# Kernel tuning notes

Hardware: AMD Instinct MI355X
Metric: run time of the kernel (lower is better)

## Reference

```python
import jax, jax.numpy as jnp
import numpy as np

B, S, E, H, L, V = 2, 2048, 512, 8, 4, 10000
D = E // H  # head_dim = 64


def _linear(x, W, b):
    # torch nn.Linear: y = x @ W.T + b, W: [out, in]
    return jnp.einsum('bse,oe->bso', x, W) + b


def _layernorm(x, g, b, eps=1e-5):
    mu = jnp.mean(x, axis=-1, keepdims=True)
    var = jnp.mean((x - mu) ** 2, axis=-1, keepdims=True)
    return (x - mu) * jax.lax.rsqrt(var + eps) * g + b


def _mha(x, Wq, bq, Wk, bk, Wv, bv, Wo, bo):
    q = _linear(x, Wq, bq).reshape(B, S, H, D).transpose(0, 2, 1, 3)
    k = _linear(x, Wk, bk).reshape(B, S, H, D).transpose(0, 2, 1, 3)
    v = _linear(x, Wv, bv).reshape(B, S, H, D).transpose(0, 2, 1, 3)
    energy = jnp.einsum('bhqd,bhkd->bhqk', q, k)  # full [B,H,S,S] scores (faithful)
    attn = jax.nn.softmax(energy / jnp.sqrt(jnp.asarray(D, x.dtype)), axis=-1)
    out = jnp.einsum('bhqk,bhkd->bhqd', attn, v)
    out = out.transpose(0, 2, 1, 3).reshape(B, S, E)
    return _linear(out, Wo, bo)


def setup_inputs() -> dict:
    key = jax.random.key(0)
    ks = jax.random.split(key, 12)
    s = 0.02
    f32 = jnp.float32
    return {
        'tokens': jax.random.randint(ks[0], (B, S), 0, V, dtype=jnp.int32),
        'embed_table': jax.random.normal(ks[1], (V, E), f32) * s,
        'pos_enc': jax.random.normal(ks[2], (1, S, E), f32) * s,
        'Wq': jax.random.normal(ks[3], (L, E, E), f32) * s,
        'bq': jnp.zeros((L, E), f32),
        'Wk': jax.random.normal(ks[4], (L, E, E), f32) * s,
        'bk': jnp.zeros((L, E), f32),
        'Wv': jax.random.normal(ks[5], (L, E, E), f32) * s,
        'bv': jnp.zeros((L, E), f32),
        'Wo': jax.random.normal(ks[6], (L, E, E), f32) * s,
        'bo': jnp.zeros((L, E), f32),
        'ln_g': jnp.ones((L, E), f32),
        'ln_b': jnp.zeros((L, E), f32),
        'Wout': jax.random.normal(ks[7], (V, E), f32) * s,
        'bout': jnp.zeros((V,), f32),
    }


def reference(tokens, embed_table, pos_enc, Wq, bq, Wk, bk, Wv, bv, Wo, bo, ln_g, ln_b, Wout, bout):
    x = embed_table[tokens] + pos_enc[:, :S, :]
    for l in range(L):
        a = _mha(x, Wq[l], bq[l], Wk[l], bk[l], Wv[l], bv[l], Wo[l], bo[l])
        x = _layernorm(x + a, ln_g[l], ln_b[l])
    # NOTE: original module defines feed_forward but never calls it in forward()
    return jnp.einsum('bse,ve->bsv', x, Wout) + bout
```

## Files before the change

### kernel.cpp

```cpp
#include <hip/hip_runtime.h>
#include <hip/hip_bf16.h>

#define Bc 2
#define Sc 2048
#define Ec 512
#define Hc 8
#define Lc 4
#define Vc 10000
#define Dc 64
#define Mc (Bc*Sc)
#define NPAD 10112
#define NROWS (16*Sc)
#define SPLITS 2

typedef __hip_bfloat16 bf16;
typedef __attribute__((ext_vector_type(8))) short frag_ab;
typedef __attribute__((ext_vector_type(4))) float frag_cd;
typedef __attribute__((ext_vector_type(16))) float f32x16;

typedef __attribute__((address_space(3))) void lds_t;
typedef __attribute__((address_space(1))) void gm_t;
static __device__ __forceinline__ void gload16(const void* g, void* l) {
  __builtin_amdgcn_global_load_lds((const gm_t*)g, (lds_t*)l, 16, 0, 0);
}
static __device__ __forceinline__ frag_ab ldfrag(const bf16* p) {
  return *(const frag_ab*)p;
}
static __device__ __forceinline__ unsigned cvtpk(float lo, float hi) {
  unsigned w;
  asm("v_cvt_pk_bf16_f32 %0, %1, %2" : "=v"(w) : "v"(lo), "v"(hi));
  return w;
}

#define SCALE2 0.18033688011112042f

#define NQKV (Lc*1536*512)
#define NO   (Lc*512*512)
#define NOUT (NPAD*512)
__global__ void convert_kernel(const float* __restrict__ Wq, const float* __restrict__ Wk,
                               const float* __restrict__ Wv, const float* __restrict__ Wo,
                               const float* __restrict__ Wout,
                               bf16* __restrict__ wqkv, bf16* __restrict__ wo,
                               bf16* __restrict__ wout) {
  long i4 = (long)(blockIdx.x * 256 + threadIdx.x) * 4;
  if (i4 >= NQKV + NO + NOUT) return;
  float4 v;
  bf16* dst;
  if (i4 < NQKV) {
    int row = (int)(i4 >> 9), colb = (int)(i4 & 511);
    int l = row / 1536, rr = row - l * 1536;
    int seg = rr >> 9, r = rr & 511;
    const float* src = (seg == 0 ? Wq : seg == 1 ? Wk : Wv) + (((long)(l * 512 + r)) << 9) + colb;
    v = *(const float4*)src;
    dst = wqkv + i4;
  } else if (i4 < NQKV + NO) {
    long j = i4 - NQKV;
    v = *(const float4*)(Wo + j);
    dst = wo + j;
  } else {
    long j = i4 - NQKV - NO;
    int row = (int)(j >> 9);
    if (row < Vc) v = *(const float4*)(Wout + j);
    else { v.x = 0.f; v.y = 0.f; v.z = 0.f; v.w = 0.f; }
    dst = wout + j;
  }
  union { bf16 h[4]; short4 s4; } u;
  u.h[0] = __float2bfloat16(v.x);
  u.h[1] = __float2bfloat16(v.y);
  u.h[2] = __float2bfloat16(v.z);
  u.h[3] = __float2bfloat16(v.w);
  *(short4*)dst = u.s4;
}

__global__ void embed_kernel(const int* __restrict__ tok, const float* __restrict__ emb,
                             const float* __restrict__ pos, float* __restrict__ x,
                             bf16* __restrict__ xb) {
  int i = blockIdx.x * 256 + threadIdx.x;
  int row = i >> 9, c = i & 511;
  int s = row & (Sc - 1);
  float v = emb[tok[row] * Ec + c] + pos[s * Ec + c];
  x[i] = v;
  xb[i] = __float2bfloat16(v);
}

template<int MODE>
__global__ __launch_bounds__(256)
void gemm_tile(const bf16* __restrict__ A, const bf16* __restrict__ W,
               const float* __restrict__ b0, const float* __restrict__ b1,
               const float* __restrict__ b2,
               void* __restrict__ o0, void* __restrict__ o1, void* __restrict__ o2) {
  __shared__ bf16 As[128 * 32];
  __shared__ bf16 Bs[128 * 32];
  const int t = threadIdx.x;
  const int lane = t & 63;
  const int wv = t >> 6;
  const int c = lane & 15, quad = lane >> 4;
  const int m0 = blockIdx.x * 128, n0 = blockIdx.y * 128;
  const int wm = (wv & 1) * 64, wn = (wv >> 1) * 64;
  frag_cd acc[4][4] = {};

  const int p0 = t, p1 = t + 256;
  const int r0 = p0 >> 2, g0 = (p0 & 3) ^ ((r0 >> 1) & 3);
  const int r1 = p1 >> 2, g1 = (p1 & 3) ^ ((r1 >> 1) & 3);
  const bf16* a0 = A + (m0 + r0) * Ec + g0 * 8;
  const bf16* a1 = A + (m0 + r1) * Ec + g1 * 8;
  const bf16* w0 = W + (n0 + r0) * Ec + g0 * 8;
  const bf16* w1 = W + (n0 + r1) * Ec + g1 * 8;

  const int sw8 = ((quad ^ ((c >> 1) & 3))) * 8;

  for (int k = 0; k < Ec; k += 32) {
    __syncthreads();
    gload16(a0 + k, As + p0 * 8);
    gload16(a1 + k, As + p1 * 8);
    gload16(w0 + k, Bs + p0 * 8);
    gload16(w1 + k, Bs + p1 * 8);
    __syncthreads();
    frag_ab af[4], bfr[4];
#pragma unroll
    for (int i = 0; i < 4; ++i)
      af[i] = *(const frag_ab*)(As + (wm + i * 16 + c) * 32 + sw8);
#pragma unroll
    for (int j = 0; j < 4; ++j)
      bfr[j] = *(const frag_ab*)(Bs + (wn + j * 16 + c) * 32 + sw8);
#pragma unroll
    for (int i = 0; i < 4; ++i)
#pragma unroll
      for (int j = 0; j < 4; ++j)
        acc[i][j] = __builtin_amdgcn_mfma_f32_16x16x32_bf16(af[i], bfr[j], acc[i][j], 0, 0, 0);
  }

#pragma unroll
  for (int j = 0; j < 4; ++j) {
    int gn = n0 + wn + j * 16 + c;
    if (MODE == 0) {
      int seg = gn >> 9, col = gn & 511;
      const float* bp = seg == 0 ? b0 : seg == 1 ? b1 : b2;
      float bias = bp[col];
      int hh = col >> 6, dd = col & 63;
#pragma unroll
      for (int i = 0; i < 4; ++i)
#pragma unroll
        for (int ii = 0; ii < 4; ++ii) {
          int gm = m0 + wm + i * 16 + quad * 4 + ii;
          int bb = gm >> 11, ss = gm & (Sc - 1);
          float v = acc[i][j][ii] + bias;
          if (seg == 0)
            ((bf16*)o0)[((((bb << 3) + hh) * Sc + ss) << 6) + dd] = __float2bfloat16(v * SCALE2);
          else if (seg == 1)
            ((bf16*)o1)[((((bb << 3) + hh) * Sc + ss) << 6) + dd] = __float2bfloat16(v);
          else
            ((bf16*)o2)[((((bb << 3) + hh) << 6) + dd) * Sc + ss] = __float2bfloat16(v);
        }
    } else if (MODE == 1) {
      float bias = b0[gn];
#pragma unroll
      for (int i = 0; i < 4; ++i)
#pragma unroll
        for (int ii = 0; ii < 4; ++ii) {
          int gm = m0 + wm + i * 16 + quad * 4 + ii;
          ((float*)o0)[((long)gm << 9) + gn] = acc[i][j][ii] + bias;
        }
    } else {
      if (gn < Vc) {
        float bias = b0[gn];
#pragma unroll
        for (int i = 0; i < 4; ++i)
#pragma unroll
          for (int ii = 0; ii < 4; ++ii) {
            int gm = m0 + wm + i * 16 + quad * 4 + ii;
            ((float*)o0)[(long)gm * Vc + gn] = acc[i][j][ii] + bias;
          }
      }
    }
  }
}

__global__ __launch_bounds__(256, 2)
void attn_kernel(const bf16* __restrict__ Q, const bf16* __restrict__ Kb,
                 const bf16* __restrict__ Vt,
                 float* __restrict__ Op, float* __restrict__ lp) {
  __shared__ bf16 Ks[2][64 * 64];
  __shared__ bf16 Vs[2][64 * 64];
  const int t = threadIdx.x;
  const int lane = t & 63, wv = t >> 6;
  const int col = lane & 31, hi = lane >> 5;
  const int col7 = col & 7;

  int wg = (blockIdx.x & 7) * 64 + (blockIdx.x >> 3);
  const int bh = wg >> 5;
  const int split = (wg >> 4) & 1;
  const int q0 = (wg & 15) * 128 + wv * 32;

  const bf16* kbase = Kb + (long)bh * Sc * Dc + (long)(split << 10) * Dc;
  const bf16* vbase = Vt + (long)bh * Dc * Sc + (split << 10);

  const int p0 = t;
  const int r0 = p0 >> 3, c0 = (p0 & 7) ^ (r0 & 7);
  const bf16* ksrc0 = kbase + r0 * Dc + c0 * 8;
  const bf16* vsrc0 = vbase + r0 * Sc + c0 * 8;

  const bf16* qp = Q + ((long)bh * Sc + q0 + col) * Dc + hi * 8;
  frag_ab qf[4];
#pragma unroll
  for (int ck = 0; ck < 4; ++ck) qf[ck] = ldfrag(qp + ck * 16);

  f32x16 o0 = {}, o1 = {};
  float lsum = 0.f;

  gload16(ksrc0, Ks[0] + p0 * 8);
  gload16(ksrc0 + 32 * Dc, Ks[0] + (p0 + 256) * 8);
  gload16(vsrc0, Vs[0] + p0 * 8);
  gload16(vsrc0 + 32 * Sc, Vs[0] + (p0 + 256) * 8);

  for (int tI = 0; tI < 16; ++tI) {
    const int cur = tI & 1;
    if (tI < 15) {
      const int k0 = (tI + 1) * 64;
      bf16* kd = Ks[cur ^ 1];
      bf16* vd = Vs[cur ^ 1];
      gload16(ksrc0 + k0 * Dc, kd + p0 * 8);
      gload16(ksrc0 + (k0 + 32) * Dc, kd + (p0 + 256) * 8);
      gload16(vsrc0 + k0, vd + p0 * 8);
      gload16(vsrc0 + k0 + 32 * Sc, vd + (p0 + 256) * 8);
      asm volatile("s_waitcnt vmcnt(4)" ::: "memory");
    } else {
      asm volatile("s_waitcnt vmcnt(0)" ::: "memory");
    }
    __builtin_amdgcn_s_barrier();
    asm volatile("" ::: "memory");

    const bf16* KsB = Ks[cur];
    const bf16* VsB = Vs[cur];

    f32x16 st0 = {}, st1 = {};
#pragma unroll
    for (int ck = 0; ck < 4; ++ck) {
      frag_ab kf0 = ldfrag(KsB + col * 64 + (((2 * ck + hi) ^ col7) << 3));
      frag_ab kf1 = ldfrag(KsB + (32 + col) * 64 + (((2 * ck + hi) ^ col7) << 3));
      st0 = __builtin_amdgcn_mfma_f32_32x32x16_bf16(kf0, qf[ck], st0, 0, 0, 0);
      st1 = __builtin_amdgcn_mfma_f32_32x32x16_bf16(kf1, qf[ck], st1, 0, 0, 0);
    }

    float pa0[16], pa1[16];
    float ls = 0.f;
#pragma unroll
    for (int r = 0; r < 16; ++r) {
      pa0[r] = exp2f(st0[r]);
      pa1[r] = exp2f(st1[r]);
      ls += pa0[r] + pa1[r];
    }
    lsum += ls;

#pragma unroll
    for (int sj = 0; sj < 4; ++sj) {
      const float* pp = (sj < 2) ? pa0 : pa1;
      const int b8 = (sj & 1) * 8;
      unsigned cw0 = cvtpk(pp[b8 + 0], pp[b8 + 1]);
      unsigned cw1 = cvtpk(pp[b8 + 2], pp[b8 + 3]);
      unsigned cw2 = cvtpk(pp[b8 + 4], pp[b8 + 5]);
      unsigned cw3 = cvtpk(pp[b8 + 6], pp[b8 + 7]);
      auto r20 = __builtin_amdgcn_permlane32_swap((int)cw2, (int)cw0, false, false);
      auto r31 = __builtin_amdgcn_permlane32_swap((int)cw3, (int)cw1, false, false);
      union { unsigned u[4]; frag_ab f; } pa;
      pa.u[0] = (unsigned)r20[1];
      pa.u[1] = (unsigned)r31[1];
      pa.u[2] = (unsigned)r20[0];
      pa.u[3] = (unsigned)r31[0];
      frag_ab vf0 = ldfrag(VsB + col * 64 + (((2 * sj + hi) ^ col7) << 3));
      frag_ab vf1 = ldfrag(VsB + (32 + col) * 64 + (((2 * sj + hi) ^ col7) << 3));
      o0 = __builtin_amdgcn_mfma_f32_32x32x16_bf16(pa.f, vf0, o0, 0, 0, 0);
      o1 = __builtin_amdgcn_mfma_f32_32x32x16_bf16(pa.f, vf1, o1, 0, 0, 0);
    }

    asm volatile("" ::: "memory");
    __builtin_amdgcn_s_barrier();
  }

  const long rbase = (long)split * NROWS + (long)bh * Sc + q0;
  float ltot = lsum + __shfl_xor(lsum, 32, 64);
  if (lane < 32) lp[rbase + col] = ltot;
#pragma unroll
  for (int r = 0; r < 16; ++r) {
    int qr = (r & 3) + 8 * (r >> 2) + 4 * hi;
    Op[(rbase + qr) * Dc + col]      = o0[r];
    Op[(rbase + qr) * Dc + col + 32] = o1[r];
  }
}

__global__ void combine_kernel(const float* __restrict__ Op, const float* __restrict__ lp,
                               bf16* __restrict__ O) {
  int t = blockIdx.x * 256 + threadIdx.x;
  int d = (t & 31) * 2, r = t >> 5;
  int bh = r >> 11, ss = r & (Sc - 1);
  float2 a = *(const float2*)(Op + (long)r * Dc + d);
  float2 b = *(const float2*)(Op + (long)(NROWS + r) * Dc + d);
  float inv = 1.f / (lp[r] + lp[NROWS + r]);
  union { bf16 h[2]; unsigned u; } u2;
  u2.h[0] = __float2bfloat16((a.x + b.x) * inv);
  u2.h[1] = __float2bfloat16((a.y + b.y) * inv);
  int bb = bh >> 3, hh = bh & 7;
  *(unsigned*)&O[((long)bb * Sc + ss) * Ec + hh * Dc + d] = u2.u;
}

__global__ void ln_kernel(const float* __restrict__ x, const float* __restrict__ a,
                          const float* __restrict__ g, const float* __restrict__ bb,
                          float* __restrict__ xo, bf16* __restrict__ xbo) {
  int lane = threadIdx.x & 63, wv = threadIdx.x >> 6;
  int row = blockIdx.x * 4 + wv;
  const float* xr = x + (long)row * Ec;
  const float* ar = a + (long)row * Ec;
  float v[8];
  float sum = 0.f;
#pragma unroll
  for (int j = 0; j < 8; ++j) {
    int c = lane + j * 64;
    v[j] = xr[c] + ar[c];
    sum += v[j];
  }
#pragma unroll
  for (int d = 1; d < 64; d <<= 1) sum += __shfl_xor(sum, d, 64);
  float mu = sum * (1.f / 512.f);
  float sq = 0.f;
#pragma unroll
  for (int j = 0; j < 8; ++j) { float t = v[j] - mu; sq += t * t; }
#pragma unroll
  for (int d = 1; d < 64; d <<= 1) sq += __shfl_xor(sq, d, 64);
  float rs = 1.f / sqrtf(sq * (1.f / 512.f) + 1e-5f);
#pragma unroll
  for (int j = 0; j < 8; ++j) {
    int c = lane + j * 64;
    float y = (v[j] - mu) * rs * g[c] + bb[c];
    xo[(long)row * Ec + c] = y;
    xbo[(long)row * Ec + c] = __float2bfloat16(y);
  }
}

extern "C" void kernel_launch(void* const* d_in, const int* in_sizes, int n_in,
                              void* d_out, int out_size, void* d_ws, size_t ws_size,
                              hipStream_t stream) {
  const int*   tokens = (const int*)d_in[0];
  const float* embed  = (const float*)d_in[1];
  const float* pos    = (const float*)d_in[2];
  const float* Wq     = (const float*)d_in[3];
  const float* bq     = (const float*)d_in[4];
  const float* Wk     = (const float*)d_in[5];
  const float* bk     = (const float*)d_in[6];
  const float* Wv     = (const float*)d_in[7];
  const float* bv     = (const float*)d_in[8];
  const float* Wo     = (const float*)d_in[9];
  const float* bo     = (const float*)d_in[10];
  const float* ln_g   = (const float*)d_in[11];
  const float* ln_b   = (const float*)d_in[12];
  const float* Wout   = (const float*)d_in[13];
  const float* bout   = (const float*)d_in[14];
  float* out = (float*)d_out;

  char* ws = (char*)d_ws;
  size_t off = 0;
  float* x_f    = (float*)(ws + off); off += (size_t)Mc * Ec * 4;
  bf16*  xb     = (bf16*)(ws + off);  off += (size_t)Mc * Ec * 2;
  float* a_f    = (float*)(ws + off); off += (size_t)Mc * Ec * 4;
  bf16*  qb     = (bf16*)(ws + off);  off += (size_t)Mc * Ec * 2;
  bf16*  kb     = (bf16*)(ws + off);  off += (size_t)Mc * Ec * 2;
  bf16*  vtb    = (bf16*)(ws + off);  off += (size_t)Mc * Ec * 2;
  bf16*  attnb  = (bf16*)(ws + off);  off += (size_t)Mc * Ec * 2;
  bf16*  wqkv_b = (bf16*)(ws + off);  off += (size_t)NQKV * 2;
  bf16*  wo_b   = (bf16*)(ws + off);  off += (size_t)NO * 2;
  bf16*  wout_b = (bf16*)(ws + off);  off += (size_t)NOUT * 2;
  float* op_f   = (float*)(ws + off); off += (size_t)SPLITS * NROWS * Dc * 4;
  float* lp_f   = (float*)(ws + off); off += (size_t)SPLITS * NROWS * 4;

  int nconv = (NQKV + NO + NOUT) / 4;
  convert_kernel<<<(nconv + 255) / 256, 256, 0, stream>>>(Wq, Wk, Wv, Wo, Wout,
                                                          wqkv_b, wo_b, wout_b);

  embed_kernel<<<(Mc * Ec) / 256, 256, 0, stream>>>(tokens, embed, pos, x_f, xb);

  dim3 gqkv(Mc / 128, 1536 / 128);
  dim3 go(Mc / 128, Ec / 128);
  for (int l = 0; l < Lc; ++l) {
    const bf16* wqkv_l = wqkv_b + (size_t)l * 1536 * Ec;
    const bf16* wo_l   = wo_b + (size_t)l * Ec * Ec;
    gemm_tile<0><<<gqkv, 256, 0, stream>>>(xb, wqkv_l, bq + l * Ec, bk + l * Ec,
                                           bv + l * Ec, qb, kb, vtb);
    attn_kernel<<<SPLITS * Hc * Bc * (Sc / 128), 256, 0, stream>>>(qb, kb, vtb,
                                                                   op_f, lp_f);
    combine_kernel<<<(NROWS * 32) / 256, 256, 0, stream>>>(op_f, lp_f, attnb);
    gemm_tile<1><<<go, 256, 0, stream>>>(attnb, wo_l, bo + l * Ec, nullptr, nullptr,
                                         a_f, nullptr, nullptr);
    ln_kernel<<<Mc / 4, 256, 0, stream>>>(x_f, a_f, ln_g + l * Ec, ln_b + l * Ec,
                                          x_f, xb);
  }

  dim3 glog(Mc / 128, NPAD / 128);
  gemm_tile<2><<<glog, 256, 0, stream>>>(xb, wout_b, bout, nullptr, nullptr,
                                         out, nullptr, nullptr);
}
```

Measured before the change: 611.2 us.

## Fuse split-attention combine into output-projection GEMM A-operand load

Removes the separate combine kernel and its bf16 attention buffer. The new o-proj GEMM reads both fp32 split partials and the softmax denominators directly, normalises them, converts to bf16 and writes the A tile to LDS. This saves one launch and a write/read round trip of the combined activations per layer. In exchange the GEMM reads fp32 data twice per element (and reloads it for each of the four N-tile blocks), and it loses the async LDS load and pipelining on the A path.

```diff
diff --git a/kernel.cpp b/kernel.cpp
--- a/kernel.cpp
+++ b/kernel.cpp
@@ -152,15 +152,6 @@
           else
             ((bf16*)o2)[((((bb << 3) + hh) << 6) + dd) * Sc + ss] = __float2bfloat16(v);
         }
-    } else if (MODE == 1) {
-      float bias = b0[gn];
-#pragma unroll
-      for (int i = 0; i < 4; ++i)
-#pragma unroll
-        for (int ii = 0; ii < 4; ++ii) {
-          int gm = m0 + wm + i * 16 + quad * 4 + ii;
-          ((float*)o0)[((long)gm << 9) + gn] = acc[i][j][ii] + bias;
-        }
     } else {
       if (gn < Vc) {
         float bias = b0[gn];
@@ -173,6 +164,92 @@
           }
       }
     }
+  }
+}
+
+__global__ __launch_bounds__(256)
+void gemm_oproj(const float* __restrict__ Op, const float* __restrict__ lp,
+                const bf16* __restrict__ W, const float* __restrict__ bias,
+                float* __restrict__ out) {
+  __shared__ bf16 As[128 * 32];
+  __shared__ bf16 Bs[128 * 32];
+  const int t = threadIdx.x;
+  const int lane = t & 63;
+  const int wv = t >> 6;
+  const int c = lane & 15, quad = lane >> 4;
+  const int m0 = blockIdx.x * 128, n0 = blockIdx.y * 128;
+  const int wm = (wv & 1) * 64, wn = (wv >> 1) * 64;
+  frag_cd acc[4][4] = {};
+
+  const int p0 = t, p1 = t + 256;
+  const int r0 = p0 >> 2, g0 = (p0 & 3) ^ ((r0 >> 1) & 3);
+  const int r1 = p1 >> 2, g1 = (p1 & 3) ^ ((r1 >> 1) & 3);
+  const int gm0 = m0 + r0, gm1 = m0 + r1;
+  const int bb0 = gm0 >> 11, ss0 = gm0 & (Sc - 1);
+  const int bb1 = gm1 >> 11, ss1 = gm1 & (Sc - 1);
+  const bf16* w0 = W + (n0 + r0) * Ec + g0 * 8;
+  const bf16* w1 = W + (n0 + r1) * Ec + g1 * 8;
+
+  const int sw8 = ((quad ^ ((c >> 1) & 3))) * 8;
+
+  for (int k = 0; k < Ec; k += 32) {
+    const int hh = k >> 6;
+    const int d00 = (k & 32) + g0 * 8;
+    const int d01 = (k & 32) + g1 * 8;
+    const long row0 = (long)((bb0 << 3) + hh) * Sc + ss0;
+    const long row1 = (long)((bb1 << 3) + hh) * Sc + ss1;
+    float4 xa0 = *(const float4*)(Op + row0 * Dc + d00);
+    float4 xa1 = *(const float4*)(Op + row0 * Dc + d00 + 4);
+    float4 ya0 = *(const float4*)(Op + (row0 + (long)NROWS) * Dc + d00);
+    float4 ya1 = *(const float4*)(Op + (row0 + (long)NROWS) * Dc + d00 + 4);
+    float4 xb0 = *(const float4*)(Op + row1 * Dc + d01);
+    float4 xb1 = *(const float4*)(Op + row1 * Dc + d01 + 4);
+    float4 yb0 = *(const float4*)(Op + (row1 + (long)NROWS) * Dc + d01);
+    float4 yb1 = *(const float4*)(Op + (row1 + (long)NROWS) * Dc + d01 + 4);
+    float inv0 = 1.f / (lp[row0] + lp[NROWS + row0]);
+    float inv1 = 1.f / (lp[row1] + lp[NROWS + row1]);
+    union { unsigned u[4]; frag_ab f; } pa0, pa1;
+    pa0.u[0] = cvtpk((xa0.x + ya0.x) * inv0, (xa0.y + ya0.y) * inv0);
+    pa0.u[1] = cvtpk((xa0.z + ya0.z) * inv0, (xa0.w + ya0.w) * inv0);
+    pa0.u[2] = cvtpk((xa1.x + ya1.x) * inv0, (xa1.y + ya1.y) * inv0);
+    pa0.u[3] = cvtpk((xa1.z + ya1.z) * inv0, (xa1.w + ya1.w) * inv0);
+    pa1.u[0] = cvtpk((xb0.x + yb0.x) * inv1, (xb0.y + yb0.y) * inv1);
+    pa1.u[1] = cvtpk((xb0.z + yb0.z) * inv1, (xb0.w + yb0.w) * inv1);
+    pa1.u[2] = cvtpk((xb1.x + yb1.x) * inv1, (xb1.y + yb1.y) * inv1);
+    pa1.u[3] = cvtpk((xb1.z + yb1.z) * inv1, (xb1.w + yb1.w) * inv1);
+
+    __syncthreads();
+    gload16(w0 + k, Bs + p0 * 8);
+    gload16(w1 + k, Bs + p1 * 8);
+    *(frag_ab*)(As + p0 * 8) = pa0.f;
+    *(frag_ab*)(As + p1 * 8) = pa1.f;
+    __syncthreads();
+
+    frag_ab af[4], bfr[4];
+#pragma unroll
+    for (int i = 0; i < 4; ++i)
+      af[i] = *(const frag_ab*)(As + (wm + i * 16 + c) * 32 + sw8);
+#pragma unroll
+    for (int j = 0; j < 4; ++j)
+      bfr[j] = *(const frag_ab*)(Bs + (wn + j * 16 + c) * 32 + sw8);
+#pragma unroll
+    for (int i = 0; i < 4; ++i)
+#pragma unroll
+      for (int j = 0; j < 4; ++j)
+        acc[i][j] = __builtin_amdgcn_mfma_f32_16x16x32_bf16(af[i], bfr[j], acc[i][j], 0, 0, 0);
+  }
+
+#pragma unroll
+  for (int j = 0; j < 4; ++j) {
+    int gn = n0 + wn + j * 16 + c;
+    float b = bias[gn];
+#pragma unroll
+    for (int i = 0; i < 4; ++i)
+#pragma unroll
+      for (int ii = 0; ii < 4; ++ii) {
+        int gm = m0 + wm + i * 16 + quad * 4 + ii;
+        out[((long)gm << 9) + gn] = acc[i][j][ii] + b;
+      }
   }
 }
 
@@ -288,21 +365,6 @@
   }
 }
 
-__global__ void combine_kernel(const float* __restrict__ Op, const float* __restrict__ lp,
-                               bf16* __restrict__ O) {
-  int t = blockIdx.x * 256 + threadIdx.x;
-  int d = (t & 31) * 2, r = t >> 5;
-  int bh = r >> 11, ss = r & (Sc - 1);
-  float2 a = *(const float2*)(Op + (long)r * Dc + d);
-  float2 b = *(const float2*)(Op + (long)(NROWS + r) * Dc + d);
-  float inv = 1.f / (lp[r] + lp[NROWS + r]);
-  union { bf16 h[2]; unsigned u; } u2;
-  u2.h[0] = __float2bfloat16((a.x + b.x) * inv);
-  u2.h[1] = __float2bfloat16((a.y + b.y) * inv);
-  int bb = bh >> 3, hh = bh & 7;
-  *(unsigned*)&O[((long)bb * Sc + ss) * Ec + hh * Dc + d] = u2.u;
-}
-
 __global__ void ln_kernel(const float* __restrict__ x, const float* __restrict__ a,
                           const float* __restrict__ g, const float* __restrict__ bb,
                           float* __restrict__ xo, bf16* __restrict__ xbo) {
@@ -364,7 +426,6 @@
   bf16*  qb     = (bf16*)(ws + off);  off += (size_t)Mc * Ec * 2;
   bf16*  kb     = (bf16*)(ws + off);  off += (size_t)Mc * Ec * 2;
   bf16*  vtb    = (bf16*)(ws + off);  off += (size_t)Mc * Ec * 2;
-  bf16*  attnb  = (bf16*)(ws + off);  off += (size_t)Mc * Ec * 2;
   bf16*  wqkv_b = (bf16*)(ws + off);  off += (size_t)NQKV * 2;
   bf16*  wo_b   = (bf16*)(ws + off);  off += (size_t)NO * 2;
   bf16*  wout_b = (bf16*)(ws + off);  off += (size_t)NOUT * 2;
@@ -386,9 +447,7 @@
                                            bv + l * Ec, qb, kb, vtb);
     attn_kernel<<<SPLITS * Hc * Bc * (Sc / 128), 256, 0, stream>>>(qb, kb, vtb,
                                                                    op_f, lp_f);
-    combine_kernel<<<(NROWS * 32) / 256, 256, 0, stream>>>(op_f, lp_f, attnb);
-    gemm_tile<1><<<go, 256, 0, stream>>>(attnb, wo_l, bo + l * Ec, nullptr, nullptr,
-                                         a_f, nullptr, nullptr);
+    gemm_oproj<<<go, 256, 0, stream>>>(op_f, lp_f, wo_l, bo + l * Ec, a_f);
     ln_kernel<<<Mc / 4, 256, 0, stream>>>(x_f, a_f, ln_g + l * Ec, ln_b + l * Ec,
                                           x_f, xb);
   }
```

Measured after the change: 636.7 us. +4.2%, slower.
